# Optimization experiments

Measured on AMD Instinct MI355X. Metric: run time of the kernel, lower is better.

Reference implementation:

```python
import jax, jax.numpy as jnp
import numpy as np

BLOCK = 128  # RHT block size (multiple of E8 lattice dim 8)


def _hadamard(n: int) -> np.ndarray:
    """Sylvester Hadamard matrix of size n (n power of 2), unnormalized."""
    H = np.array([[1.0]], dtype=np.float32)
    while H.shape[0] < n:
        H = np.block([[H, H], [H, -H]]).astype(np.float32)
    return H

_H = jnp.asarray(_hadamard(BLOCK) / np.sqrt(BLOCK))  # orthonormal [BLOCK, BLOCK]


def rht(x, signs):
    """Block-diagonal randomized Hadamard transform: x*signs then blockwise H.
    x: [T, D] with D % BLOCK == 0; signs: [D] of +-1."""
    T, D = x.shape
    xs = (x * signs).reshape(T, D // BLOCK, BLOCK)
    return jnp.einsum('tnb,bc->tnc', xs, _H).reshape(T, D)


def e8rht_linear(x, wq, scale, signs):
    """E8RHT quantized linear: rotate input, dequantize weight, matmul.
    wq: [out, in] quantized codes (stored as float), scale: [out] per-row scale."""
    xr = rht(x, signs)                       # [T, in]
    w = wq * scale[:, None]                  # dequantize [out, in]
    return xr @ w.T                          # [T, out]


def setup_inputs() -> dict:
    key = jax.random.key(0)
    ks = jax.random.split(key, 7)
    T, D_IN, D_MID, D_OUT = 16384, 1024, 4096, 1024
    x = jax.random.normal(ks[0], (T, D_IN), dtype=jnp.float32)
    # simulate lattice-quantized codes: small-integer-ish values
    up_wq = jnp.round(jax.random.normal(ks[1], (D_MID, D_IN)) * 2.0)
    up_scale = (jax.random.uniform(ks[2], (D_MID,)) * 0.02 + 0.005).astype(jnp.float32)
    down_wq = jnp.round(jax.random.normal(ks[3], (D_OUT, D_MID)) * 2.0)
    down_scale = (jax.random.uniform(ks[4], (D_OUT,)) * 0.02 + 0.005).astype(jnp.float32)
    up_signs = jnp.sign(jax.random.normal(ks[5], (D_IN,))).astype(jnp.float32)
    down_signs = jnp.sign(jax.random.normal(ks[6], (D_MID,))).astype(jnp.float32)
    return {"x": x, "up_wq": up_wq, "up_scale": up_scale,
            "down_wq": down_wq, "down_scale": down_scale,
            "up_signs": up_signs, "down_signs": down_signs}


def reference(x, up_wq, up_scale, down_wq, down_scale, up_signs, down_signs):
    h = e8rht_linear(x, up_wq, up_scale, up_signs)       # [T, D_MID]
    a = jax.nn.gelu(h)                                    # non-gated activation
    out = e8rht_linear(a, down_wq, down_scale, down_signs)  # [T, D_OUT]
    return out
```

## Files before the change

### kernel.cpp

```cpp
#include <hip/hip_runtime.h>
#include <stdint.h>


typedef __attribute__((ext_vector_type(8))) short short8;
typedef __attribute__((ext_vector_type(4))) float floatx4;

#define GLOAD(gp, lp)                                                               \
  __builtin_amdgcn_global_load_lds(                                                 \
      (const __attribute__((address_space(1))) unsigned int*)(gp),                  \
      (__attribute__((address_space(3))) unsigned int*)(lp), 16, 0, 0)

#define SCHED0() __builtin_amdgcn_sched_barrier(0)
#define BARRIER()                                  \
  do {                                             \
    SCHED0();                                      \
    asm volatile("" ::: "memory");                 \
    __builtin_amdgcn_s_barrier();                  \
    asm volatile("" ::: "memory");                 \
    SCHED0();                                      \
  } while (0)
#define LGKM0()                                              \
  do {                                                       \
    asm volatile("s_waitcnt lgkmcnt(0)" ::: "memory");       \
    SCHED0();                                                \
  } while (0)
#define LGKM_HINT() asm volatile("s_waitcnt lgkmcnt(8)" ::: "memory")
#define VMCNT(n)                                             \
  do {                                                       \
    asm volatile("s_waitcnt vmcnt(" #n ")" ::: "memory");    \
    SCHED0();                                                \
  } while (0)

__device__ __forceinline__ float bf2f(unsigned int u16) {
    union { unsigned int i; float f; } v;
    v.i = u16 << 16;
    return v.f;
}

__device__ __forceinline__ unsigned short f2bf(float f) {
    union { float f; unsigned int i; } v;
    v.f = f;
    unsigned int r = v.i + 0x7FFFu + ((v.i >> 16) & 1u);
    return (unsigned short)(r >> 16);
}

__device__ __forceinline__ float gelu_tanh(float x) {
    float u = 0.7978845608028654f * (x + 0.044715f * x * x * x);
    float e = __expf(2.0f * u);
    float t = 1.0f - 2.0f / (e + 1.0f);
    return 0.5f * x * (1.0f + t);
}

__device__ __forceinline__ int dtype_flag(const void* signs_raw) {
    return ((*(const unsigned int*)signs_raw) & 0xFFFFu) ? 1 : 0;
}

__device__ __forceinline__ void fwht_block(const void* wq, const void* scale,
                                           const void* signs, unsigned short* out,
                                           int fl, int D, int nblk, int gwave, int lane) {
    int o = gwave / nblk;
    int blk = gwave - o * nblk;
    size_t base = (size_t)o * D + (size_t)blk * 128;

    float v0, v1, s0, s1, sc;
    if (fl) {
        unsigned int p = ((const unsigned int*)((const unsigned short*)wq + base))[lane];
        v0 = bf2f(p & 0xffffu);
        v1 = bf2f(p >> 16);
        unsigned int sp =
            ((const unsigned int*)((const unsigned short*)signs + (size_t)blk * 128))[lane];
        s0 = bf2f(sp & 0xffffu);
        s1 = bf2f(sp >> 16);
        sc = bf2f(((const unsigned short*)scale)[o]);
    } else {
        const float* wf = (const float*)wq + base;
        v0 = wf[2 * lane];
        v1 = wf[2 * lane + 1];
        const float* sf = (const float*)signs + (size_t)blk * 128;
        s0 = sf[2 * lane];
        s1 = sf[2 * lane + 1];
        sc = ((const float*)scale)[o];
    }

    {
        float a = v0, b = v1;
        v0 = a + b;
        v1 = a - b;
    }
#pragma unroll
    for (int m = 1; m <= 32; m <<= 1) {
        float p0 = __shfl_xor(v0, m, 64);
        float p1 = __shfl_xor(v1, m, 64);
        if (lane & m) {
            v0 = p0 - v0;
            v1 = p1 - v1;
        } else {
            v0 = v0 + p0;
            v1 = v1 + p1;
        }
    }

    sc *= 0.08838834764831845f;
    unsigned short o0 = f2bf(v0 * sc * s0);
    unsigned short o1 = f2bf(v1 * sc * s1);
    ((unsigned int*)(out + base))[lane] = (unsigned int)o0 | ((unsigned int)o1 << 16);
}

__global__ __launch_bounds__(256) void prep(const void* __restrict__ x,
                                            const void* __restrict__ up_wq,
                                            const void* __restrict__ up_scale,
                                            const void* __restrict__ dn_wq,
                                            const void* __restrict__ dn_scale,
                                            const void* __restrict__ up_signs,
                                            const void* __restrict__ dn_signs,
                                            unsigned short* __restrict__ x_bf,
                                            unsigned short* __restrict__ w_up,
                                            unsigned short* __restrict__ w_dn,
                                            int nbX, int nbW, int D_IN, int D_MID) {
    const int fl = dtype_flag(up_signs);
    const int bid = blockIdx.x;
    if (bid < nbX) {
        size_t e = ((size_t)bid * 256 + threadIdx.x) * 8;
        if (fl) {
            *(uint4*)(x_bf + e) = *(const uint4*)((const unsigned short*)x + e);
        } else {
            const float* xf = (const float*)x + e;
            uint4 r;
            r.x = (unsigned)f2bf(xf[0]) | ((unsigned)f2bf(xf[1]) << 16);
            r.y = (unsigned)f2bf(xf[2]) | ((unsigned)f2bf(xf[3]) << 16);
            r.z = (unsigned)f2bf(xf[4]) | ((unsigned)f2bf(xf[5]) << 16);
            r.w = (unsigned)f2bf(xf[6]) | ((unsigned)f2bf(xf[7]) << 16);
            *(uint4*)(x_bf + e) = r;
        }
    } else if (bid < nbX + nbW) {
        int gwave = (bid - nbX) * 4 + (threadIdx.x >> 6);
        fwht_block(up_wq, up_scale, up_signs, w_up, fl, D_IN, D_IN / 128, gwave,
                   threadIdx.x & 63);
    } else {
        int gwave = (bid - nbX - nbW) * 4 + (threadIdx.x >> 6);
        fwht_block(dn_wq, dn_scale, dn_signs, w_dn, fl, D_MID, D_MID / 128, gwave,
                   threadIdx.x & 63);
    }
}

__device__ __forceinline__ void stage_half(const unsigned short* g, unsigned short* l,
                                           size_t goff, int K, int ldsW) {
    GLOAD(g + goff, l + ldsW);
    GLOAD(g + goff + (size_t)8 * K, l + ldsW + 512);
}

__device__ __forceinline__ void ld_frags(short8 (&fr)[2][2], const unsigned short* base,
                                         int o0, int o1) {
#pragma unroll
    for (int f = 0; f < 2; ++f) {
        fr[f][0] = *(const short8*)(base + f * 1024 + o0);
        fr[f][1] = *(const short8*)(base + f * 1024 + o1);
    }
}

__device__ __forceinline__ void ld_frags4(short8 (&fr)[4][2], const unsigned short* base,
                                          int o0, int o1) {
#pragma unroll
    for (int f = 0; f < 4; ++f) {
        fr[f][0] = *(const short8*)(base + f * 1024 + o0);
        fr[f][1] = *(const short8*)(base + f * 1024 + o1);
    }
}

__device__ __forceinline__ void mfma_quad(floatx4 (&acc)[8][4], const short8 (&ar)[4][2],
                                          const short8 (&br)[2][2], int MO, int NO) {
    __builtin_amdgcn_s_setprio(1);
#pragma unroll
    for (int ks = 0; ks < 2; ++ks)
#pragma unroll
        for (int fm = 0; fm < 4; ++fm)
#pragma unroll
            for (int fn = 0; fn < 2; ++fn)
                acc[MO + fm][NO + fn] = __builtin_amdgcn_mfma_f32_16x16x32_bf16(
                    ar[fm][ks], br[fn][ks], acc[MO + fm][NO + fn], 0, 0, 0);
    __builtin_amdgcn_s_setprio(0);
}

template <int ACT, int OUT_DYN>
__global__ __launch_bounds__(512, 2) void gemm256(const unsigned short* __restrict__ A,
                                                  const unsigned short* __restrict__ B,
                                                  void* __restrict__ C,
                                                  const void* __restrict__ sflag,
                                                  int N, int K, int rowOff,
                                                  int NTn, int GM, int strip) {
    __shared__ __align__(16) unsigned short As[2][2][128 * 64];
    __shared__ __align__(16) unsigned short Bs[2][2][128 * 64];

    int flat = blockIdx.x;
    int mt, nt;
    if (strip > 0) {
        int xcd = flat & 7;
        int s = flat >> 3;
        int perPanel = GM * NTn;
        int p = s / perPanel;
        int r = s - p * perPanel;
        nt = r / GM;
        mt = xcd * strip + p * GM + (r - nt * GM);
    } else {
        int perPanel = GM * NTn;
        int p = flat / perPanel;
        int r = flat - p * perPanel;
        nt = r / GM;
        mt = p * GM + (r - nt * GM);
    }
    const int tileM = mt * 256, tileN = nt * 256;

    const int tid = threadIdx.x;
    const int lane = tid & 63;
    const int wave = tid >> 6;
    const int wm = wave >> 2;
    const int wn = wave & 3;

    int fl = 1;
    if (OUT_DYN) {
        fl = dtype_flag(sflag);
        asm volatile("" ::"v"(fl));
    }

    const int gcol = (((lane & 7) ^ (lane >> 3)) * 8);
    const size_t goff = (size_t)(wave * 16 + (lane >> 3)) * K + gcol;
    const int ldsW = wave * 1024;

    const int sw = (lane & 7) * 8;
    const int o0 = (lane & 15) * 64 + (((lane >> 4) * 8) ^ sw);
    const int o1 = (lane & 15) * 64 + ((32 | ((lane >> 4) * 8)) ^ sw);

    const unsigned short* Ab = A + (size_t)tileM * K;
    const unsigned short* Bb = B + (size_t)tileN * K;
    const int NTt = K >> 6;

    floatx4 acc[8][4];
#pragma unroll
    for (int i = 0; i < 8; ++i)
#pragma unroll
        for (int j = 0; j < 4; ++j) acc[i][j] = (floatx4)0.0f;

    stage_half(Ab, &As[0][0][0], goff, K, ldsW);
    stage_half(Bb, &Bs[0][0][0], goff, K, ldsW);
    stage_half(Ab + (size_t)128 * K, &As[0][1][0], goff, K, ldsW);
    stage_half(Bb + (size_t)128 * K, &Bs[0][1][0], goff, K, ldsW);
    if (NTt > 1) {
        stage_half(Ab + 64, &As[1][0][0], goff, K, ldsW);
        stage_half(Bb + 64, &Bs[1][0][0], goff, K, ldsW);
        VMCNT(4);
    } else {
        VMCNT(0);
    }
    BARRIER();

    short8 ar0[4][2], ar1[4][2], br0[2][2], br1[2][2];

    for (int t = 0; t < NTt; ++t) {
        const int d = t & 1, e = d ^ 1;
        const unsigned short* Ah = &As[d][wm][0];
        const unsigned short* Bh = &Bs[d][wn >> 1][0];
        const int bro = (wn & 1) * 64 * 64;

        ld_frags4(ar0, Ah, o0, o1);
        ld_frags(br0, Bh + bro, o0, o1);
        if (t + 1 < NTt)
            stage_half(Ab + (size_t)128 * K + (size_t)(t + 1) * 64, &As[e][1][0], goff, K,
                       ldsW);
        LGKM_HINT();
        BARRIER();
        LGKM0();
        mfma_quad(acc, ar0, br0, 0, 0);
        BARRIER();

        ld_frags4(ar1, Ah + 64 * 64, o0, o1);
        ld_frags(br1, Bh + bro + 32 * 64, o0, o1);
        if (t + 1 < NTt)
            stage_half(Bb + (size_t)128 * K + (size_t)(t + 1) * 64, &Bs[e][1][0], goff, K,
                       ldsW);
        LGKM_HINT();
        BARRIER();
        LGKM0();
        mfma_quad(acc, ar1, br0, 4, 0);
        BARRIER();

        if (t + 2 < NTt)
            stage_half(Ab + (size_t)(t + 2) * 64, &As[d][0][0], goff, K, ldsW);
        BARRIER();
        mfma_quad(acc, ar1, br1, 4, 2);
        BARRIER();

        if (t + 2 < NTt) {
            stage_half(Bb + (size_t)(t + 2) * 64, &Bs[d][0][0], goff, K, ldsW);
            VMCNT(4);
        } else {
            VMCNT(0);
        }
        BARRIER();
        mfma_quad(acc, ar0, br1, 0, 2);
        BARRIER();
    }

    const int c4 = lane & 15;
    const int rg = (lane >> 4) * 4;
#pragma unroll
    for (int fm = 0; fm < 8; ++fm) {
        const int gr = tileM + wm * 128 + fm * 16 + rg;
#pragma unroll
        for (int fn = 0; fn < 4; ++fn) {
            const int gc = tileN + wn * 64 + fn * 16 + c4;
#pragma unroll
            for (int j = 0; j < 4; ++j) {
                float v = acc[fm][fn][j];
                if (ACT) v = gelu_tanh(v);
                size_t idx = (size_t)(rowOff + gr + j) * N + gc;
                if (fl)
                    ((unsigned short*)C)[idx] = f2bf(v);
                else
                    ((float*)C)[idx] = v;
            }
        }
    }
}

static inline int div_le(int n, int cap) {
    for (int g = cap; g > 1; --g)
        if (n % g == 0) return g;
    return 1;
}

extern "C" void kernel_launch(void* const* d_in, const int* in_sizes, int n_in,
                              void* d_out, int out_size, void* d_ws, size_t ws_size,
                              hipStream_t stream) {
    const int T = 16384, D_IN = 1024, D_MID = 4096, D_OUT = 1024;

    unsigned short* w_up = (unsigned short*)d_ws;
    unsigned short* w_dn = w_up + (size_t)D_MID * D_IN;
    unsigned short* x_bf = w_dn + (size_t)D_OUT * D_MID;
    unsigned short* a_buf = x_bf + (size_t)T * D_IN;

    size_t used = ((size_t)D_MID * D_IN + (size_t)D_OUT * D_MID + (size_t)T * D_IN) * 2;
    size_t avail = ws_size > used ? ws_size - used : 0;
    long tc = (long)(avail / ((size_t)D_MID * 2));
    tc = (tc / 256) * 256;
    if (tc > T) tc = T;
    if (tc < 256) tc = 256;
    const int Tc = (int)tc;

    {
        int nbX = (T * D_IN / 8) / 256;
        int nbW = (D_MID * (D_IN / 128)) / 4;
        prep<<<dim3(nbX + 2 * nbW), dim3(256), 0, stream>>>(
            d_in[0], d_in[1], d_in[2], d_in[3], d_in[4], d_in[5], d_in[6], x_bf, w_up, w_dn,
            nbX, nbW, D_IN, D_MID);
    }

    for (int r0 = 0; r0 < T; r0 += Tc) {
        int Ms = (T - r0 < Tc) ? (T - r0) : Tc;
        int MT = Ms / 256;
        int strip = (MT % 8 == 0 && MT >= 8) ? MT / 8 : 0;

        {
            int NTn = D_MID / 256;
            int GM = (strip > 0) ? div_le(strip, 4) : div_le(MT, 4);
            gemm256<1, 0><<<dim3(MT * NTn), dim3(512), 0, stream>>>(
                x_bf + (size_t)r0 * D_IN, w_up, a_buf, d_in[5], D_MID, D_IN, 0, NTn, GM,
                strip);
        }
        {
            int NTn = D_OUT / 256;
            int GM = (strip > 0) ? div_le(strip, 2) : div_le(MT, 2);
            gemm256<0, 1><<<dim3(MT * NTn), dim3(512), 0, stream>>>(
                a_buf, w_dn, d_out, d_in[5], D_OUT, D_MID, r0, NTn, GM, strip);
        }
    }
}
```

Measured before the change: 426.0 us.

## Software-pipeline LDS fragment loads across MFMA phases and halve barriers in GEMM loop

Restructures the main K loop so each phase's LDS fragment reads are issued ahead of the MFMA block that uses them. The next iteration's ar0/br0 fragments are prefetched during the last MFMA quad, and partial lgkmcnt waits replace full drains. Per-iteration barriers drop from eight to four, and global staging pointers are advanced incrementally rather than recomputed. This aims to hide LDS latency behind matrix math and cut synchronisation stalls. It relies on the fragment-buffer reuse ordering being correct across the reduced barriers.

```diff
diff --git a/kernel.cpp b/kernel.cpp
--- a/kernel.cpp
+++ b/kernel.cpp
@@ -19,12 +19,11 @@
     asm volatile("" ::: "memory");                 \
     SCHED0();                                      \
   } while (0)
-#define LGKM0()                                              \
+#define LGKM(n)                                              \
   do {                                                       \
-    asm volatile("s_waitcnt lgkmcnt(0)" ::: "memory");       \
+    asm volatile("s_waitcnt lgkmcnt(" #n ")" ::: "memory");  \
     SCHED0();                                                \
   } while (0)
-#define LGKM_HINT() asm volatile("s_waitcnt lgkmcnt(8)" ::: "memory")
 #define VMCNT(n)                                             \
   do {                                                       \
     asm volatile("s_waitcnt vmcnt(" #n ")" ::: "memory");    \
@@ -214,6 +213,7 @@
     const int lane = tid & 63;
     const int wave = tid >> 6;
     const int wm = wave >> 2;
+    const int wh = (wave >> 1) & 1;
     const int wn = wave & 3;
 
     int fl = 1;
@@ -229,6 +229,7 @@
     const int sw = (lane & 7) * 8;
     const int o0 = (lane & 15) * 64 + (((lane >> 4) * 8) ^ sw);
     const int o1 = (lane & 15) * 64 + ((32 | ((lane >> 4) * 8)) ^ sw);
+    const int bro = (wn & 1) * 64 * 64;
 
     const unsigned short* Ab = A + (size_t)tileM * K;
     const unsigned short* Bb = B + (size_t)tileN * K;
@@ -254,50 +255,55 @@
     BARRIER();
 
     short8 ar0[4][2], ar1[4][2], br0[2][2], br1[2][2];
+    ld_frags4(ar0, &As[0][wm][0], o0, o1);
+    ld_frags(br0, &Bs[0][wh][0] + bro, o0, o1);
+    SCHED0();
+
+    const unsigned short* pA1 = Ab + (size_t)128 * K + 64;
+    const unsigned short* pB1 = Bb + (size_t)128 * K + 64;
+    const unsigned short* pA0 = Ab + 128;
+    const unsigned short* pB0 = Bb + 128;
 
     for (int t = 0; t < NTt; ++t) {
         const int d = t & 1, e = d ^ 1;
         const unsigned short* Ah = &As[d][wm][0];
-        const unsigned short* Bh = &Bs[d][wn >> 1][0];
-        const int bro = (wn & 1) * 64 * 64;
-
-        ld_frags4(ar0, Ah, o0, o1);
-        ld_frags(br0, Bh + bro, o0, o1);
-        if (t + 1 < NTt)
-            stage_half(Ab + (size_t)128 * K + (size_t)(t + 1) * 64, &As[e][1][0], goff, K,
-                       ldsW);
-        LGKM_HINT();
+        const unsigned short* Bh = &Bs[d][wh][0] + bro;
+
+        if (t + 1 < NTt) stage_half(pA1, &As[e][1][0], goff, K, ldsW);
+        ld_frags4(ar1, Ah + 4096, o0, o1);
+        LGKM(8);
         BARRIER();
-        LGKM0();
         mfma_quad(acc, ar0, br0, 0, 0);
+
+        if (t + 1 < NTt) stage_half(pB1, &Bs[e][1][0], goff, K, ldsW);
+        ld_frags(br1, Bh + 2048, o0, o1);
+        LGKM(4);
         BARRIER();
-
-        ld_frags4(ar1, Ah + 64 * 64, o0, o1);
-        ld_frags(br1, Bh + bro + 32 * 64, o0, o1);
-        if (t + 1 < NTt)
-            stage_half(Bb + (size_t)128 * K + (size_t)(t + 1) * 64, &Bs[e][1][0], goff, K,
-                       ldsW);
-        LGKM_HINT();
+        mfma_quad(acc, ar1, br0, 4, 0);
+
+        if (t + 2 < NTt) stage_half(pA0, &As[d][0][0], goff, K, ldsW);
+        LGKM(0);
         BARRIER();
-        LGKM0();
-        mfma_quad(acc, ar1, br0, 4, 0);
-        BARRIER();
-
-        if (t + 2 < NTt)
-            stage_half(Ab + (size_t)(t + 2) * 64, &As[d][0][0], goff, K, ldsW);
-        BARRIER();
-        mfma_quad(acc, ar1, br1, 4, 2);
-        BARRIER();
+        mfma_quad(acc, ar0, br1, 0, 2);
 
         if (t + 2 < NTt) {
-            stage_half(Bb + (size_t)(t + 2) * 64, &Bs[d][0][0], goff, K, ldsW);
+            stage_half(pB0, &Bs[d][0][0], goff, K, ldsW);
             VMCNT(4);
         } else {
             VMCNT(0);
         }
         BARRIER();
-        mfma_quad(acc, ar0, br1, 0, 2);
-        BARRIER();
+        if (t + 1 < NTt) {
+            ld_frags4(ar0, &As[e][wm][0], o0, o1);
+            ld_frags(br0, &Bs[e][wh][0] + bro, o0, o1);
+            SCHED0();
+        }
+        mfma_quad(acc, ar1, br1, 4, 2);
+
+        pA1 += 64;
+        pB1 += 64;
+        pA0 += 64;
+        pB0 += 64;
     }
 
     const int c4 = lane & 15;
```

New measurement: 500.1 us. 17.4% more time.
